# Kernel optimization log

Hardware: AMD Instinct MI355X
Metric: run time of the kernel (lower is better)

## Reference

```python
import jax, jax.numpy as jnp
import numpy as np

B, N, E = 4, 10000, 160000
IN, HEADS, C = 128, 4, 64  # hidden_dim=64, num_heads=4 -> per-layer out = 256
OUT = HEADS * C
NEG_SLOPE = 0.2  # PyG GATConv default leaky_relu slope


def setup_inputs() -> dict:
    key = jax.random.key(0)
    ks = jax.random.split(key, 10)
    x = jax.random.normal(ks[0], (B, N, IN), dtype=jnp.float32)
    edge_index = jax.random.randint(ks[1], (2, E), 0, N, dtype=jnp.int64)
    s = 0.05
    W1 = jax.random.normal(ks[2], (IN, OUT), dtype=jnp.float32) * s
    a_src1 = jax.random.normal(ks[3], (HEADS, C), dtype=jnp.float32) * s
    a_dst1 = jax.random.normal(ks[4], (HEADS, C), dtype=jnp.float32) * s
    b1 = jnp.zeros((OUT,), dtype=jnp.float32)
    W2 = jax.random.normal(ks[5], (OUT, OUT), dtype=jnp.float32) * s
    a_src2 = jax.random.normal(ks[6], (HEADS, C), dtype=jnp.float32) * s
    a_dst2 = jax.random.normal(ks[7], (HEADS, C), dtype=jnp.float32) * s
    b2 = jnp.zeros((OUT,), dtype=jnp.float32)
    return {"x": x, "edge_index": edge_index,
            "W1": W1, "a_src1": a_src1, "a_dst1": a_dst1, "b1": b1,
            "W2": W2, "a_src2": a_src2, "a_dst2": a_dst2, "b2": b2}


def _gat_layer(h, W, a_src, a_dst, b, src, dst, n_nodes):
    # h: [N, in_dim]; src/dst: [E'] (self-loops included)
    hW = (h @ W).reshape(n_nodes, HEADS, C)            # [N, H, C]
    al_src = jnp.sum(hW * a_src, axis=-1)              # [N, H]
    al_dst = jnp.sum(hW * a_dst, axis=-1)              # [N, H]
    e = jax.nn.leaky_relu(al_src[src] + al_dst[dst], NEG_SLOPE)  # [E', H]
    # segment softmax over edges grouped by destination node
    m = jax.ops.segment_max(e, dst, num_segments=n_nodes)        # [N, H]
    ex = jnp.exp(e - m[dst])                                     # [E', H]
    denom = jax.ops.segment_sum(ex, dst, num_segments=n_nodes)   # [N, H]
    alpha = ex / (denom[dst] + 1e-16)                            # [E', H]
    out = jax.ops.segment_sum(alpha[:, :, None] * hW[src], dst, num_segments=n_nodes)  # [N, H, C]
    return out.reshape(n_nodes, OUT) + b


def reference(x, edge_index, W1, a_src1, a_dst1, b1, W2, a_src2, a_dst2, b2):
    n_nodes = x.shape[1]
    loops = jnp.arange(n_nodes, dtype=edge_index.dtype)
    src = jnp.concatenate([edge_index[0], loops])  # PyG GATConv adds self-loops
    dst = jnp.concatenate([edge_index[1], loops])

    def per_graph(xb):
        h = jax.nn.elu(_gat_layer(xb, W1, a_src1, a_dst1, b1, src, dst, n_nodes))
        h = jax.nn.elu(_gat_layer(h, W2, a_src2, a_dst2, b2, src, dst, n_nodes))
        return h  # dropout is identity in eval mode

    return jax.vmap(per_graph)(x)  # [B, N, OUT]
```

## Files before the change

kernel.cpp:

```cpp
#include <hip/hip_runtime.h>
#include <hip/hip_fp16.h>
#include <math.h>

#define NNODES 10000
#define NB 4
#define NIN 128
#define NOUT 256
#define NHEADS 4
#define NE 160000
#define NEP (NE + NNODES)
#define NEG_SLOPE 0.2f
#define MTOT (NB * NNODES)
#define MPAD 40064
#define DMAX 96

typedef _Float16 f16;
typedef f16 f16x4 __attribute__((ext_vector_type(4)));
typedef f16 f16x8 __attribute__((ext_vector_type(8)));
typedef float f32x4 __attribute__((ext_vector_type(4)));

typedef __attribute__((address_space(1))) const void* gas_p;
typedef __attribute__((address_space(3))) void* las_p;

__device__ __forceinline__ float lrelu(float x) { return x >= 0.f ? x : NEG_SLOPE * x; }

__device__ __forceinline__ __half2 h2shfl_xor(__half2 v, int off) {
  union { __half2 h; int i; } u;
  u.h = v;
  u.i = __shfl_xor(u.i, off, 64);
  return u.h;
}


#define NXV (MTOT * NIN / 4)
#define CVT_ITEMS (NXV + NIN * NOUT + NOUT * NOUT)

__global__ void cvt_scatter_kernel(const float* __restrict__ x,
                                   const float* __restrict__ W1,
                                   const float* __restrict__ W2,
                                   const int* __restrict__ ei,
                                   f16* __restrict__ x16,
                                   f16* __restrict__ W1t,
                                   f16* __restrict__ W2t,
                                   int* __restrict__ cnt,
                                   int* __restrict__ csr) {
  int t = blockIdx.x * blockDim.x + threadIdx.x;
  if (t < NEP) {
    int s, d;
    if (t < NE) { s = ei[t]; d = ei[NE + t]; } else { s = t - NE; d = s; }
    int pos = atomicAdd(&cnt[d], 1);
    if (pos < DMAX) csr[d * DMAX + pos] = s;
  }
  int i = t;
  if (i < NXV) {
    float4 v = ((const float4*)x)[i];
    f16x4 o = {(f16)v.x, (f16)v.y, (f16)v.z, (f16)v.w};
    *((f16x4*)x16 + i) = o;
    return;
  }
  i -= NXV;
  if (i < NIN * NOUT) {
    int k = i >> 8, c = i & 255;
    W1t[c * NIN + k] = (f16)W1[i];
    return;
  }
  i -= NIN * NOUT;
  if (i < NOUT * NOUT) {
    int k = i >> 8, c = i & 255;
    W2t[c * NOUT + k] = (f16)W2[i];
  }
}


template<int K>
__global__ __launch_bounds__(256) void mfma_gemm(const f16* __restrict__ A,
                                                 const f16* __restrict__ Bt,
                                                 f16* __restrict__ C,
                                                 const float* __restrict__ a_src,
                                                 const float* __restrict__ a_dst,
                                                 float* __restrict__ alS,
                                                 float* __restrict__ alD) {
  __shared__ f16 As[128 * 32];
  __shared__ f16 Bs[128 * 32];
  const int tid  = threadIdx.x;
  const int lane = tid & 63;
  const int wid  = tid >> 6;
  const int bm = blockIdx.x * 128;
  const int bn = blockIdx.y * 128;
  const int wr = (wid >> 1) * 64;
  const int wc = (wid & 1) * 64;
  f32x4 acc[4][4] = {};

  const int srow   = lane >> 2;
  const int schnk0 = lane & 3;

  for (int k0 = 0; k0 < K; k0 += 32) {
    #pragma unroll
    for (int t = 0; t < 2; ++t) {
      int rb  = wid * 32 + t * 16;
      int row = rb + srow;
      int sc  = schnk0 ^ ((row >> 1) & 3);
      __builtin_amdgcn_global_load_lds((gas_p)(A  + (size_t)(bm + row) * K + k0 + sc * 8),
                                       (las_p)(As + rb * 32), 16, 0, 0);
      __builtin_amdgcn_global_load_lds((gas_p)(Bt + (size_t)(bn + row) * K + k0 + sc * 8),
                                       (las_p)(Bs + rb * 32), 16, 0, 0);
    }
    __syncthreads();

    f16x8 av[4], bv[4];
    const int fr = lane & 15;
    const int kc = lane >> 4;
    #pragma unroll
    for (int i = 0; i < 4; ++i) {
      int ra = wr + i * 16 + fr;
      av[i] = *(const f16x8*)(As + ra * 32 + ((kc ^ ((ra >> 1) & 3)) * 8));
      int rb2 = wc + i * 16 + fr;
      bv[i] = *(const f16x8*)(Bs + rb2 * 32 + ((kc ^ ((rb2 >> 1) & 3)) * 8));
    }
    #pragma unroll
    for (int i = 0; i < 4; ++i)
      #pragma unroll
      for (int j = 0; j < 4; ++j)
        acc[i][j] = __builtin_amdgcn_mfma_f32_16x16x32_f16(av[i], bv[j], acc[i][j], 0, 0, 0);
    __syncthreads();
  }

  const int fr = lane & 15;
  const int rg = lane >> 4;
  #pragma unroll
  for (int i = 0; i < 4; ++i)
    #pragma unroll
    for (int r = 0; r < 4; ++r) {
      size_t row = bm + wr + i * 16 + rg * 4 + r;
      #pragma unroll
      for (int j = 0; j < 4; ++j) {
        int col = bn + wc + j * 16 + fr;
        C[row * NOUT + col] = (f16)acc[i][j][r];
      }
    }

  const int hb = (bn + wc) >> 6;
  float aS[4], aD[4];
  #pragma unroll
  for (int j = 0; j < 4; ++j) {
    int c = hb * 64 + j * 16 + fr;
    aS[j] = a_src[c];
    aD[j] = a_dst[c];
  }
  float sS[4][4], sD[4][4];
  #pragma unroll
  for (int i = 0; i < 4; ++i)
    #pragma unroll
    for (int r = 0; r < 4; ++r) {
      float vS = 0.f, vD = 0.f;
      #pragma unroll
      for (int j = 0; j < 4; ++j) {
        vS = fmaf(acc[i][j][r], aS[j], vS);
        vD = fmaf(acc[i][j][r], aD[j], vD);
      }
      sS[i][r] = vS;
      sD[i][r] = vD;
    }
  #pragma unroll
  for (int off = 1; off < 16; off <<= 1)
    #pragma unroll
    for (int i = 0; i < 4; ++i)
      #pragma unroll
      for (int r = 0; r < 4; ++r) {
        sS[i][r] += __shfl_xor(sS[i][r], off, 64);
        sD[i][r] += __shfl_xor(sD[i][r], off, 64);
      }
  if (fr == 0) {
    #pragma unroll
    for (int i = 0; i < 4; ++i)
      #pragma unroll
      for (int r = 0; r < 4; ++r) {
        size_t row = bm + wr + i * 16 + rg * 4 + r;
        if (row < MTOT) {
          alS[row * 4 + hb] = sS[i][r];
          alD[row * 4 + hb] = sD[i][r];
        }
      }
  }
}


template<bool F16OUT>
__global__ __launch_bounds__(256) void gat_edge_kernel(
    const f16* __restrict__ hW, const float* __restrict__ alS,
    const float* __restrict__ alD, const int* __restrict__ cnt,
    const int* __restrict__ csr, const float* __restrict__ bias,
    float* __restrict__ outF, f16* __restrict__ outH) {
  __shared__ float lds[4][256];
  const int bid  = blockIdx.x;
  const int xcd  = bid & 7;
  const int b    = xcd >> 1;
  const int l    = (bid >> 3) * 2 + (xcd & 1);
  const int slot = (int)threadIdx.x >> 6;
  const int node = l * 4 + slot;
  const int lane = (int)threadIdx.x & 63;

  const f16*   hWb  = hW  + (size_t)b * NNODES * NOUT;
  const float* alSb = alS + (size_t)b * NNODES * NHEADS;
  const float* alDb = alD + (size_t)b * NNODES * NHEADS;
  const int deg  = min(cnt[node], DMAX);
  const int base = node * DMAX;

  const int k3  = lane >> 4;
  const int sub = lane & 15;
  const int hh  = sub >> 2;
  const float dh = alDb[node * 4 + hh];

  float s = 0.f;
  __half2 acc2[8];
  #pragma unroll
  for (int q = 0; q < 8; ++q) acc2[q] = __float2half2_rn(0.f);

  for (int idx = k3; idx < deg; idx += 4) {
    int u = csr[base + idx];
    float e  = lrelu(alSb[u * 4 + hh] + dh);
    float pp = __expf(fminf(e, 60.f));
    s += pp;
    __half2 a2 = __float2half2_rn(pp);
    const __half2* cp = (const __half2*)(hWb + (size_t)u * NOUT + sub * 16);
    #pragma unroll
    for (int q = 0; q < 8; ++q)
      acc2[q] = __hfma2(a2, cp[q], acc2[q]);
  }

  #pragma unroll
  for (int off = 16; off < 64; off <<= 1) {
    s += __shfl_xor(s, off, 64);
    #pragma unroll
    for (int q = 0; q < 8; ++q)
      acc2[q] = __hadd2(acc2[q], h2shfl_xor(acc2[q], off));
  }
  const float inv = 1.0f / (s + 1e-16f);

  if (k3 == 0) {
    #pragma unroll
    for (int q = 0; q < 8; ++q) {
      float2 f = __half22float2(acc2[q]);
      lds[slot][sub * 16 + q * 2]     = f.x * inv;
      lds[slot][sub * 16 + q * 2 + 1] = f.y * inv;
    }
  }
  __syncthreads();

  float4 r = *(const float4*)&lds[slot][lane * 4];
  float4 bb = *(const float4*)(bias + lane * 4);
  r.x += bb.x; r.y += bb.y; r.z += bb.z; r.w += bb.w;
  r.x = r.x > 0.f ? r.x : (__expf(r.x) - 1.f);
  r.y = r.y > 0.f ? r.y : (__expf(r.y) - 1.f);
  r.z = r.z > 0.f ? r.z : (__expf(r.z) - 1.f);
  r.w = r.w > 0.f ? r.w : (__expf(r.w) - 1.f);

  const size_t o = ((size_t)b * NNODES + node) * NOUT + lane * 4;
  if (F16OUT) {
    f16x4 hv = {(f16)r.x, (f16)r.y, (f16)r.z, (f16)r.w};
    *(f16x4*)(outH + o) = hv;
  } else {
    *(float4*)(outF + o) = r;
  }
}


extern "C" void kernel_launch(void* const* d_in, const int* in_sizes, int n_in,
                              void* d_out, int out_size, void* d_ws, size_t ws_size,
                              hipStream_t stream) {
  const float* x   = (const float*)d_in[0];
  const int*   ei  = (const int*)d_in[1];
  const float* W1  = (const float*)d_in[2];
  const float* as1 = (const float*)d_in[3];
  const float* ad1 = (const float*)d_in[4];
  const float* b1  = (const float*)d_in[5];
  const float* W2  = (const float*)d_in[6];
  const float* as2 = (const float*)d_in[7];
  const float* ad2 = (const float*)d_in[8];
  const float* b2  = (const float*)d_in[9];
  float* out = (float*)d_out;

  char* p = (char*)d_ws;
  auto carve = [&](size_t bytes) -> void* {
    void* q = (void*)p;
    p += (bytes + 255) & ~(size_t)255;
    return q;
  };
  int*   cnt    = (int*)carve((size_t)NNODES * 4);
  int*   csr    = (int*)carve((size_t)NNODES * DMAX * 4);
  f16*   hW16   = (f16*)carve((size_t)MPAD * NOUT * 2);
  float* alS    = (float*)carve((size_t)MTOT * NHEADS * 4);
  float* alD    = (float*)carve((size_t)MTOT * NHEADS * 4);
  f16*   W1t    = (f16*)carve((size_t)NOUT * NIN * 2);
  f16*   W2t    = (f16*)carve((size_t)NOUT * NOUT * 2);

  f16* x16 = (f16*)d_out;
  f16* h1  = (f16*)((char*)d_out + (size_t)MPAD * NIN * 2);

  hipMemsetAsync(cnt, 0, (size_t)NNODES * 4, stream);
  cvt_scatter_kernel<<<(CVT_ITEMS + 255) / 256, 256, 0, stream>>>(x, W1, W2, ei,
                                                                  x16, W1t, W2t,
                                                                  cnt, csr);

  dim3 ggrid(MPAD / 128, NOUT / 128);

  mfma_gemm<NIN><<<ggrid, 256, 0, stream>>>(x16, W1t, hW16, as1, ad1, alS, alD);
  gat_edge_kernel<true><<<NNODES, 256, 0, stream>>>(hW16, alS, alD, cnt, csr, b1, nullptr, h1);

  mfma_gemm<NOUT><<<ggrid, 256, 0, stream>>>(h1, W2t, hW16, as2, ad2, alS, alD);
  gat_edge_kernel<false><<<NNODES, 256, 0, stream>>>(hW16, alS, alD, cnt, csr, b2, out, nullptr);
}
```

Baseline: 217.0 us.

## Precompute per-edge attention weights in LDS, then gather with more edges in flight

The edge kernel now runs in two phases. First, each (edge, head) score and exponential is computed once by a 16-edge by 4-head lane layout, and the weights and source indices are stored in shared memory. Then the weighted feature aggregation runs in two half-channel passes with 8 edges processed concurrently per wave instead of 4. This removes the redundant per-lane exp and score work and aims to hide more gather latency, at the cost of extra LDS traffic, a second loop pass and extra shuffle reductions.

```diff
diff --git a/kernel.cpp b/kernel.cpp
--- a/kernel.cpp
+++ b/kernel.cpp
@@ -191,6 +191,8 @@
     const float* __restrict__ alD, const int* __restrict__ cnt,
     const int* __restrict__ csr, const float* __restrict__ bias,
     float* __restrict__ outF, f16* __restrict__ outH) {
+  __shared__ float p_lds[4][DMAX][4];
+  __shared__ int   u_lds[4][DMAX];
   __shared__ float lds[4][256];
   const int bid  = blockIdx.x;
   const int xcd  = bid & 7;
@@ -206,43 +208,54 @@
   const int deg  = min(cnt[node], DMAX);
   const int base = node * DMAX;
 
-  const int k3  = lane >> 4;
-  const int sub = lane & 15;
-  const int hh  = sub >> 2;
-  const float dh = alDb[node * 4 + hh];
-
+  const int h1 = lane & 3;
+  const int es = lane >> 2;
+  const float ald1 = alDb[node * 4 + h1];
   float s = 0.f;
-  __half2 acc2[8];
-  #pragma unroll
-  for (int q = 0; q < 8; ++q) acc2[q] = __float2half2_rn(0.f);
-
-  for (int idx = k3; idx < deg; idx += 4) {
+  for (int idx = es; idx < deg; idx += 16) {
     int u = csr[base + idx];
-    float e  = lrelu(alSb[u * 4 + hh] + dh);
+    float e  = lrelu(alSb[u * 4 + h1] + ald1);
     float pp = __expf(fminf(e, 60.f));
+    p_lds[slot][idx][h1] = pp;
+    if (h1 == 0) u_lds[slot][idx] = u;
     s += pp;
-    __half2 a2 = __float2half2_rn(pp);
-    const __half2* cp = (const __half2*)(hWb + (size_t)u * NOUT + sub * 16);
-    #pragma unroll
-    for (int q = 0; q < 8; ++q)
-      acc2[q] = __hfma2(a2, cp[q], acc2[q]);
-  }
-
-  #pragma unroll
-  for (int off = 16; off < 64; off <<= 1) {
-    s += __shfl_xor(s, off, 64);
-    #pragma unroll
-    for (int q = 0; q < 8; ++q)
-      acc2[q] = __hadd2(acc2[q], h2shfl_xor(acc2[q], off));
-  }
-  const float inv = 1.0f / (s + 1e-16f);
-
-  if (k3 == 0) {
-    #pragma unroll
-    for (int q = 0; q < 8; ++q) {
-      float2 f = __half22float2(acc2[q]);
-      lds[slot][sub * 16 + q * 2]     = f.x * inv;
-      lds[slot][sub * 16 + q * 2 + 1] = f.y * inv;
+  }
+  #pragma unroll
+  for (int off = 4; off < 64; off <<= 1) s += __shfl_xor(s, off, 64);
+
+  const int k8  = lane >> 3;
+  const int sub = lane & 7;
+  #pragma unroll
+  for (int cc = 0; cc < 2; ++cc) {
+    const int hh = cc * 2 + (sub >> 2);
+    __half2 acc2[8];
+    #pragma unroll
+    for (int q = 0; q < 8; ++q) acc2[q] = __float2half2_rn(0.f);
+
+    for (int idx = k8; idx < deg; idx += 8) {
+      int u    = u_lds[slot][idx];
+      float pp = p_lds[slot][idx][hh];
+      __half2 a2 = __float2half2_rn(pp);
+      const __half2* cp = (const __half2*)(hWb + (size_t)u * NOUT + cc * 128 + sub * 16);
+      #pragma unroll
+      for (int q = 0; q < 8; ++q)
+        acc2[q] = __hfma2(a2, cp[q], acc2[q]);
+    }
+
+    #pragma unroll
+    for (int off = 8; off < 64; off <<= 1)
+      #pragma unroll
+      for (int q = 0; q < 8; ++q)
+        acc2[q] = __hadd2(acc2[q], h2shfl_xor(acc2[q], off));
+
+    if (k8 == 0) {
+      const float invh = 1.0f / (__shfl(s, hh, 64) + 1e-16f);
+      #pragma unroll
+      for (int q = 0; q < 8; ++q) {
+        float2 f = __half22float2(acc2[q]);
+        lds[slot][cc * 128 + sub * 16 + q * 2]     = f.x * invh;
+        lds[slot][cc * 128 + sub * 16 + q * 2 + 1] = f.y * invh;
+      }
     }
   }
   __syncthreads();
```

New measurement: 225.7 us. 4.0% more time.

## Assign one node per block and stage edge weights in shared memory for aggregation

Applied to the files above, without the earlier changes.

The edge kernel now processes one (batch, node) per 256-thread block instead of four nodes per block, and the grid grows to match. A first phase computes the exp attention scores for all edges of the node at once (one thread per edge-head) and stores them with the neighbour ids in LDS, reducing the softmax denominator across waves. A second phase has each wave handle one head's 64 channels with 16 edge streams, using 16-byte vector loads of neighbour features, then applies bias and ELU and writes directly. This removes the redundant per-stream score recomputation and widens the parallelism per node, at the cost of four times more blocks, an extra barrier, and leaving only a quarter of the lanes active in the epilogue.

```diff
diff --git a/kernel.cpp b/kernel.cpp
--- a/kernel.cpp
+++ b/kernel.cpp
@@ -191,14 +191,16 @@
     const float* __restrict__ alD, const int* __restrict__ cnt,
     const int* __restrict__ csr, const float* __restrict__ bias,
     float* __restrict__ outF, f16* __restrict__ outH) {
-  __shared__ float lds[4][256];
+  __shared__ float p_lds[DMAX][4];
+  __shared__ int   u_lds[DMAX];
+  __shared__ float s_part[4][4];
   const int bid  = blockIdx.x;
   const int xcd  = bid & 7;
   const int b    = xcd >> 1;
-  const int l    = (bid >> 3) * 2 + (xcd & 1);
-  const int slot = (int)threadIdx.x >> 6;
-  const int node = l * 4 + slot;
-  const int lane = (int)threadIdx.x & 63;
+  const int node = (bid >> 3) * 2 + (xcd & 1);
+  const int tid  = (int)threadIdx.x;
+  const int wid  = tid >> 6;
+  const int lane = tid & 63;
 
   const f16*   hWb  = hW  + (size_t)b * NNODES * NOUT;
   const float* alSb = alS + (size_t)b * NNODES * NHEADS;
@@ -206,61 +208,78 @@
   const int deg  = min(cnt[node], DMAX);
   const int base = node * DMAX;
 
-  const int k3  = lane >> 4;
-  const int sub = lane & 15;
-  const int hh  = sub >> 2;
-  const float dh = alDb[node * 4 + hh];
-
+  const int h1 = tid & 3;
+  const int es = tid >> 2;
+  const float ald1 = alDb[node * 4 + h1];
   float s = 0.f;
+  for (int idx = es; idx < deg; idx += 64) {
+    int u = csr[base + idx];
+    float e  = lrelu(alSb[u * 4 + h1] + ald1);
+    float pp = __expf(fminf(e, 60.f));
+    p_lds[idx][h1] = pp;
+    if (h1 == 0) u_lds[idx] = u;
+    s += pp;
+  }
+  #pragma unroll
+  for (int off = 4; off < 64; off <<= 1) s += __shfl_xor(s, off, 64);
+  if (lane < 4) s_part[wid][lane] = s;
+  __syncthreads();
+  const float stot = s_part[0][wid] + s_part[1][wid] + s_part[2][wid] + s_part[3][wid];
+  const float inv = 1.0f / (stot + 1e-16f);
+
+  const int strm = lane >> 2;
+  const int sub  = lane & 3;
+  const int ch0  = wid * 64 + sub * 16;
   __half2 acc2[8];
   #pragma unroll
   for (int q = 0; q < 8; ++q) acc2[q] = __float2half2_rn(0.f);
 
-  for (int idx = k3; idx < deg; idx += 4) {
-    int u = csr[base + idx];
-    float e  = lrelu(alSb[u * 4 + hh] + dh);
-    float pp = __expf(fminf(e, 60.f));
-    s += pp;
+  for (int idx = strm; idx < deg; idx += 16) {
+    int u    = u_lds[idx];
+    float pp = p_lds[idx][wid];
     __half2 a2 = __float2half2_rn(pp);
-    const __half2* cp = (const __half2*)(hWb + (size_t)u * NOUT + sub * 16);
+    const __half2* cp = (const __half2*)(hWb + (size_t)u * NOUT + ch0);
+    __half2 d[8];
+    *(uint4*)&d[0] = *(const uint4*)&cp[0];
+    *(uint4*)&d[4] = *(const uint4*)&cp[4];
     #pragma unroll
     for (int q = 0; q < 8; ++q)
-      acc2[q] = __hfma2(a2, cp[q], acc2[q]);
-  }
-
-  #pragma unroll
-  for (int off = 16; off < 64; off <<= 1) {
-    s += __shfl_xor(s, off, 64);
+      acc2[q] = __hfma2(a2, d[q], acc2[q]);
+  }
+
+  #pragma unroll
+  for (int off = 4; off < 64; off <<= 1)
     #pragma unroll
     for (int q = 0; q < 8; ++q)
       acc2[q] = __hadd2(acc2[q], h2shfl_xor(acc2[q], off));
-  }
-  const float inv = 1.0f / (s + 1e-16f);
-
-  if (k3 == 0) {
+
+  if (strm == 0) {
+    float v[16];
     #pragma unroll
     for (int q = 0; q < 8; ++q) {
       float2 f = __half22float2(acc2[q]);
-      lds[slot][sub * 16 + q * 2]     = f.x * inv;
-      lds[slot][sub * 16 + q * 2 + 1] = f.y * inv;
-    }
-  }
-  __syncthreads();
-
-  float4 r = *(const float4*)&lds[slot][lane * 4];
-  float4 bb = *(const float4*)(bias + lane * 4);
-  r.x += bb.x; r.y += bb.y; r.z += bb.z; r.w += bb.w;
-  r.x = r.x > 0.f ? r.x : (__expf(r.x) - 1.f);
-  r.y = r.y > 0.f ? r.y : (__expf(r.y) - 1.f);
-  r.z = r.z > 0.f ? r.z : (__expf(r.z) - 1.f);
-  r.w = r.w > 0.f ? r.w : (__expf(r.w) - 1.f);
-
-  const size_t o = ((size_t)b * NNODES + node) * NOUT + lane * 4;
-  if (F16OUT) {
-    f16x4 hv = {(f16)r.x, (f16)r.y, (f16)r.z, (f16)r.w};
-    *(f16x4*)(outH + o) = hv;
-  } else {
-    *(float4*)(outF + o) = r;
+      v[q * 2]     = f.x * inv;
+      v[q * 2 + 1] = f.y * inv;
+    }
+    const float* bp = bias + ch0;
+    #pragma unroll
+    for (int j = 0; j < 16; ++j) {
+      float r = v[j] + bp[j];
+      v[j] = r > 0.f ? r : (__expf(r) - 1.f);
+    }
+    const size_t o = ((size_t)b * NNODES + node) * NOUT + ch0;
+    if (F16OUT) {
+      f16x8 h0, h1v;
+      #pragma unroll
+      for (int j = 0; j < 8; ++j) { h0[j] = (f16)v[j]; h1v[j] = (f16)v[8 + j]; }
+      *(f16x8*)(outH + o)     = h0;
+      *(f16x8*)(outH + o + 8) = h1v;
+    } else {
+      #pragma unroll
+      for (int q = 0; q < 4; ++q)
+        *(float4*)(outF + o + q * 4) =
+            make_float4(v[q * 4], v[q * 4 + 1], v[q * 4 + 2], v[q * 4 + 3]);
+    }
   }
 }
 
@@ -305,8 +324,8 @@
   dim3 ggrid(MPAD / 128, NOUT / 128);
 
   mfma_gemm<NIN><<<ggrid, 256, 0, stream>>>(x16, W1t, hW16, as1, ad1, alS, alD);
-  gat_edge_kernel<true><<<NNODES, 256, 0, stream>>>(hW16, alS, alD, cnt, csr, b1, nullptr, h1);
+  gat_edge_kernel<true><<<MTOT, 256, 0, stream>>>(hW16, alS, alD, cnt, csr, b1, nullptr, h1);
 
   mfma_gemm<NOUT><<<ggrid, 256, 0, stream>>>(h1, W2t, hW16, as2, ad2, alS, alD);
-  gat_edge_kernel<false><<<NNODES, 256, 0, stream>>>(hW16, alS, alD, cnt, csr, b2, out, nullptr);
-}
+  gat_edge_kernel<false><<<MTOT, 256, 0, stream>>>(hW16, alS, alD, cnt, csr, b2, out, nullptr);
+}
```

After: 311.2 us. 1.43x slower.
